# Kernel optimization log

Measured on AMD Instinct MI355X. Metric: run time of the kernel, lower is better.

Reference implementation:

```python
import jax, jax.numpy as jnp
import numpy as np
from jax import lax

OBS_LEN = 8
PRED_LEN = 12
DIM = 128      # hidden_dim
EMB = 64       # embedding_dim
HEADS = 4
MODES = 5
SCENE = 32     # peds per scene
NPED = 8192    # total peds (256 scenes)


def _lin(key, out_d, in_d):
    kw, kb = jax.random.split(key)
    w = jax.random.normal(kw, (out_d, in_d), jnp.float32) / np.sqrt(in_d).astype(np.float32)
    b = jax.random.normal(kb, (out_d,), jnp.float32) * 0.01
    return w, b


def _stack(key, n, out_d, in_d):
    ws, bs = zip(*[_lin(k, out_d, in_d) for k in jax.random.split(key, n)])
    return jnp.stack(ws), jnp.stack(bs)


def setup_inputs() -> dict:
    key = jax.random.key(0)
    ks = jax.random.split(key, 24)
    inp = {}
    inp['obs_traj'] = jax.random.normal(ks[0], (OBS_LEN, NPED, 2), jnp.float32)
    inp['pe_w'], inp['pe_b'] = _lin(ks[1], EMB, 2)
    inp['lstm_wih'], inp['lstm_bih'] = _lin(ks[2], 4 * DIM, EMB)
    inp['lstm_whh'], inp['lstm_bhh'] = _lin(ks[3], 4 * DIM, DIM)
    inp['rp_w1'], inp['rp_b1'] = _lin(ks[4], DIM // 2, 2)
    inp['rp_w2'], inp['rp_b2'] = _lin(ks[5], DIM, DIM // 2)
    inp['wq'], inp['bq'] = _lin(ks[6], DIM, DIM)
    inp['wk'], inp['bk'] = _lin(ks[7], DIM, DIM)
    inp['wv'], inp['bv'] = _lin(ks[8], DIM, DIM)
    inp['wo'], inp['bo'] = _lin(ks[9], DIM, DIM)
    inp['op_w'], inp['op_b'] = _lin(ks[10], DIM, 2 * DIM)
    inp['mp_w1'], inp['mp_b1'] = _lin(ks[11], DIM, 2 * DIM)
    inp['mp_w2'], inp['mp_b2'] = _lin(ks[12], MODES, DIM)
    inp['td_w1'], inp['td_b1'] = _stack(ks[13], MODES, DIM, 2 * DIM)
    inp['td_w2'], inp['td_b2'] = _stack(ks[14], MODES, DIM, DIM)
    inp['td_w3'], inp['td_b3'] = _stack(ks[15], MODES, PRED_LEN * 2, DIM)
    inp['ud_w1'], inp['ud_b1'] = _stack(ks[16], MODES, DIM // 2, 2 * DIM)
    inp['ud_w2'], inp['ud_b2'] = _stack(ks[17], MODES, PRED_LEN * 2, DIM // 2)
    inp['scene_size'] = SCENE
    return inp


def reference(obs_traj, pe_w, pe_b, lstm_wih, lstm_bih, lstm_whh, lstm_bhh,
              rp_w1, rp_b1, rp_w2, rp_b2, wq, bq, wk, bk, wv, bv, wo, bo,
              op_w, op_b, mp_w1, mp_b1, mp_w2, mp_b2,
              td_w1, td_b1, td_w2, td_b2, td_w3, td_b3,
              ud_w1, ud_b1, ud_w2, ud_b2, scene_size):
    obs = jnp.transpose(obs_traj, (1, 0, 2))          # (N, T, 2)
    N = obs.shape[0]
    D = lstm_whh.shape[1]

    # ---- NodeHistoryEncoder: Linear embed + 1-layer LSTM, last hidden ----
    emb = jnp.einsum('ntd,ed->nte', obs, pe_w) + pe_b  # (N, T, EMB)

    def step(carry, x):
        h, c = carry
        g = x @ lstm_wih.T + lstm_bih + h @ lstm_whh.T + lstm_bhh
        i, f, gg, o = jnp.split(g, 4, axis=-1)          # torch gate order i,f,g,o
        c = jax.nn.sigmoid(f) * c + jax.nn.sigmoid(i) * jnp.tanh(gg)
        h = jax.nn.sigmoid(o) * jnp.tanh(c)
        return (h, c), None

    h0 = jnp.zeros((N, D), obs.dtype)
    (node_features, _), _ = lax.scan(step, (h0, h0), jnp.swapaxes(emb, 0, 1))
    last_pos = obs[:, -1, :]                            # (N, 2)

    # ---- EdgeEncoder: per-scene rel-pos-biased multi-head attention ----
    S = scene_size
    B = N // S
    feat = node_features.reshape(B, S, D)
    pos = last_pos.reshape(B, S, 2)
    rel = pos[:, None, :, :] - pos[:, :, None, :]       # [b,i,j] = pos_j - pos_i
    rel_enc = jax.nn.relu(jnp.einsum('bijd,hd->bijh', rel, rp_w1) + rp_b1)
    rel_enc = jnp.einsum('bijh,eh->bije', rel_enc, rp_w2) + rp_b2  # (B,S,S,D)
    kv = feat[:, None, :, :] + rel_enc                  # key == value
    dh = D // HEADS
    q = (feat @ wq.T + bq).reshape(B, S, HEADS, dh)
    kp = (jnp.einsum('bijd,ed->bije', kv, wk) + bk).reshape(B, S, S, HEADS, dh)
    vp = (jnp.einsum('bijd,ed->bije', kv, wv) + bv).reshape(B, S, S, HEADS, dh)
    scores = jnp.einsum('bihd,bijhd->bhij', q, kp) / np.sqrt(dh).astype(np.float32)
    attn = jax.nn.softmax(scores, axis=-1)
    ctx = jnp.einsum('bhij,bijhd->bihd', attn, vp).reshape(B, S, D)
    attn_out = ctx @ wo.T + bo
    edge = (jnp.concatenate([feat, attn_out], axis=-1) @ op_w.T + op_b).reshape(N, D)

    f_all = jnp.concatenate([node_features, edge], axis=-1)  # (N, 2D)

    # ---- GMMDecoder ----
    probs = jax.nn.softmax(jax.nn.relu(f_all @ mp_w1.T + mp_b1) @ mp_w2.T + mp_b2, axis=-1)
    h1 = jax.nn.relu(jnp.einsum('nd,mhd->nmh', f_all, td_w1) + td_b1)    # (N,M,D)
    h2 = jax.nn.relu(jnp.einsum('nmh,mgh->nmg', h1, td_w2) + td_b2)
    traj = (jnp.einsum('nmg,mog->nmo', h2, td_w3) + td_b3).reshape(N, MODES, PRED_LEN, 2)
    u1 = jax.nn.relu(jnp.einsum('nd,mhd->nmh', f_all, ud_w1) + ud_b1)
    sigmas = jax.nn.softplus(jnp.einsum('nmh,moh->nmo', u1, ud_w2) + ud_b2).reshape(N, MODES, PRED_LEN, 2)
    predictions = jnp.cumsum(traj, axis=2) + last_pos[:, None, None, :]
    return predictions, probs
```

## Files before the change

### kernel.cpp

```cpp
#include <hip/hip_runtime.h>
#include <math.h>

typedef __attribute__((ext_vector_type(8))) short short8;
typedef __attribute__((ext_vector_type(4))) float f32x4;

#define NPED 8192
#define INVS 0.1767766952966369f

#define B_WHH    0
#define B_WQKV   131072
#define B_WK2PAD 229376
#define B_OPWE   294912
#define B_MPW1   360448
#define B_TDW1   425984
#define B_TDW2   753664
#define B_TDW3C  917504
#define F_WIHE   958464
#define F_BEFF   962560
#define F_WV2T   964608
#define F_BQKV   997376
#define F_BEDGE  998912
#define F_TDB3C  999424
#define F_ZERO   999936
#define A_FEAT   1000960
#define A_QKV    3098112

__device__ __forceinline__ float bf2f(ushort u) {
  union { unsigned i; float f; } v; v.i = ((unsigned)u) << 16; return v.f;
}
__device__ __forceinline__ float blo(unsigned u) {
  union { unsigned i; float f; } v; v.i = u << 16; return v.f;
}
__device__ __forceinline__ float bhi(unsigned u) {
  union { unsigned i; float f; } v; v.i = u & 0xffff0000u; return v.f;
}
__device__ __forceinline__ ushort f2bf(float f) {
  union { float f; unsigned i; } v; v.f = f;
  unsigned r = v.i + 0x7fffu + ((v.i >> 16) & 1u);
  return (ushort)(r >> 16);
}

__global__ __launch_bounds__(256) void prep(
    const float* __restrict__ wih, const float* __restrict__ bih, const float* __restrict__ bhh,
    const float* __restrict__ pew, const float* __restrict__ peb,
    const float* __restrict__ wk, const float* __restrict__ wv,
    const float* __restrict__ rpw2, const float* __restrict__ rpb2,
    const float* __restrict__ bq, const float* __restrict__ bk, const float* __restrict__ bv,
    const float* __restrict__ whh, const float* __restrict__ wq, const float* __restrict__ wo,
    const float* __restrict__ opw, const float* __restrict__ opb, const float* __restrict__ bo,
    const float* __restrict__ mpw1,
    const float* __restrict__ tdw1, const float* __restrict__ tdw2,
    const float* __restrict__ tdw3, const float* __restrict__ tdb3,
    char* __restrict__ wsb) {
  int tid = blockIdx.x * 256 + threadIdx.x;
  if (tid < 512) {
    int d = tid;
    float s0 = 0.f, s1 = 0.f, sb = 0.f;
    for (int e = 0; e < 64; ++e) {
      float w = wih[d * 64 + e];
      s0 += w * pew[e * 2]; s1 += w * pew[e * 2 + 1]; sb += w * peb[e];
    }
    ((float*)(wsb + F_WIHE))[d * 2] = s0;
    ((float*)(wsb + F_WIHE))[d * 2 + 1] = s1;
    ((float*)(wsb + F_BEFF))[d] = bih[d] + bhh[d] + sb;
  } else if (tid < 49664) {
    int j = tid - 512; int n = j >> 7, k = j & 127;
    float v = (n < 128) ? wq[n * 128 + k] * INVS
                        : (n < 256) ? wk[(n - 128) * 128 + k] : wv[(n - 256) * 128 + k];
    ((ushort*)(wsb + B_WQKV))[j] = f2bf(v);
  } else if (tid < 82432) {
    int idx = tid - 49664; int r = idx >> 7, d = idx & 127;
    int h = r >> 6, e = r & 63;
    float s = 0.f;
    if ((d >> 5) == h)
      for (int c = 0; c < 128; ++c) s += wk[d * 128 + c] * rpw2[c * 64 + e];
    ((ushort*)(wsb + B_WK2PAD))[idx] = f2bf(s);
  } else if (tid < 115200) {
    int idx = tid - 82432; int o = idx >> 8, k = idx & 255;
    float s;
    if (k < 128) s = opw[o * 256 + k];
    else {
      s = 0.f;
      for (int c = 0; c < 128; ++c) s += opw[o * 256 + 128 + c] * wo[c * 128 + (k - 128)];
    }
    ((ushort*)(wsb + B_OPWE))[idx] = f2bf(s);
  } else if (tid < 147968) {
    int j = tid - 115200; ((ushort*)(wsb + B_MPW1))[j] = f2bf(mpw1[j]);
  } else if (tid < 311808) {
    int j = tid - 147968; ((ushort*)(wsb + B_TDW1))[j] = f2bf(tdw1[j]);
  } else if (tid < 393728) {
    int j = tid - 311808; ((ushort*)(wsb + B_TDW2))[j] = f2bf(tdw2[j]);
  } else if (tid < 414208) {
    int j = tid - 393728; int m = j >> 12, r = j & 4095, o = r >> 7, k = r & 127;
    float s = 0.f;
    if (o < 24) {
      int c = o & 1, jj = o >> 1;
      for (int jp = 0; jp <= jj; ++jp) s += tdw3[(m * 24 + jp * 2 + c) * 128 + k];
    }
    ((ushort*)(wsb + B_TDW3C))[j] = f2bf(s);
  } else if (tid < 414328) {
    int j = tid - 414208; int m = j / 24, o = j % 24;
    int c = o & 1, jj = o >> 1;
    float s = 0.f;
    for (int jp = 0; jp <= jj; ++jp) s += tdb3[m * 24 + jp * 2 + c];
    ((float*)(wsb + F_TDB3C))[j] = s;
  } else if (tid < 414712) {
    int d = tid - 414328;
    float s;
    if (d < 128) s = bq[d] * INVS;
    else if (d < 256) {
      int dd = d - 128; s = bk[dd];
      for (int c = 0; c < 128; ++c) s += wk[dd * 128 + c] * rpb2[c];
    } else {
      int dd = d - 256; s = bv[dd];
      for (int c = 0; c < 128; ++c) s += wv[dd * 128 + c] * rpb2[c];
    }
    ((float*)(wsb + F_BQKV))[d] = s;
  } else if (tid < 414840) {
    int o = tid - 414712;
    float s = opb[o];
    for (int c = 0; c < 128; ++c) s += opw[o * 256 + 128 + c] * bo[c];
    ((float*)(wsb + F_BEDGE))[o] = s;
  } else if (tid < 415096) {
    ((float*)(wsb + F_ZERO))[tid - 414840] = 0.f;
  } else if (tid < 423288) {
    int idx = tid - 415096; int e = idx >> 7, hd = idx & 127;
    float s = 0.f;
    for (int c = 0; c < 128; ++c) s += wv[hd * 128 + c] * rpw2[c * 64 + e];
    ((float*)(wsb + F_WV2T))[idx] = s;
  } else if (tid < 488824) {
    int i = tid - 423288;
    ((ushort*)(wsb + B_WHH))[i] = f2bf(whh[i]);
  }
}

__global__ __launch_bounds__(512) void lstm_mfma(
    const float* __restrict__ obs, const ushort* __restrict__ whhb,
    const float* __restrict__ wihe, const float* __restrict__ beff,
    ushort* __restrict__ feat) {
  __shared__ ushort Hs[32 * 128];
  __shared__ float obs_s[8][32][2];
  int tid = threadIdx.x;
  int w = tid >> 6, l = tid & 63;
  int lm = l & 15, lg = l >> 4;
  int nb = blockIdx.x * 32;
  {
    int ts = tid >> 6, p = (tid >> 1) & 31, c = tid & 1;
    obs_s[ts][p][c] = obs[ts * (NPED * 2) + (nb + p) * 2 + c];
  }
  for (int i = tid; i < 4096; i += 512) Hs[i] = 0;
  short8 bfr[4][4];
  float wx0[4], wx1[4], be[4];
#pragma unroll
  for (int q = 0; q < 4; ++q) {
    int g = q * 128 + w * 16 + lm;
    wx0[q] = wihe[g * 2]; wx1[q] = wihe[g * 2 + 1]; be[q] = beff[g];
#pragma unroll
    for (int ks = 0; ks < 4; ++ks)
      bfr[q][ks] = *(const short8*)(const void*)&whhb[g * 128 + ks * 32 + lg * 8];
  }
  float cst[2][4] = {};
  __syncthreads();
  for (int ts = 0; ts < 8; ++ts) {
    f32x4 acc[2][4];
#pragma unroll
    for (int mi = 0; mi < 2; ++mi)
#pragma unroll
      for (int r = 0; r < 4; ++r) {
        int p = mi * 16 + lg * 4 + r;
        float ox = obs_s[ts][p][0], oy = obs_s[ts][p][1];
#pragma unroll
        for (int q = 0; q < 4; ++q)
          acc[mi][q][r] = be[q] + wx0[q] * ox + wx1[q] * oy;
      }
#pragma unroll
    for (int ks = 0; ks < 4; ++ks) {
      int p0 = lm, p1 = 16 + lm;
      short8 a0 = *(const short8*)(const void*)&Hs[p0 * 128 + ((ks * 32 + lg * 8) ^ ((p0 & 7) << 3))];
      short8 a1 = *(const short8*)(const void*)&Hs[p1 * 128 + ((ks * 32 + lg * 8) ^ ((p1 & 7) << 3))];
#pragma unroll
      for (int q = 0; q < 4; ++q) {
        acc[0][q] = __builtin_amdgcn_mfma_f32_16x16x32_bf16(a0, bfr[q][ks], acc[0][q], 0, 0, 0);
        acc[1][q] = __builtin_amdgcn_mfma_f32_16x16x32_bf16(a1, bfr[q][ks], acc[1][q], 0, 0, 0);
      }
    }
    __syncthreads();
    int d = w * 16 + lm;
#pragma unroll
    for (int mi = 0; mi < 2; ++mi)
#pragma unroll
      for (int r = 0; r < 4; ++r) {
        int p = mi * 16 + lg * 4 + r;
        float xi = acc[mi][0][r], xf = acc[mi][1][r], xg = acc[mi][2][r], xo = acc[mi][3][r];
        float ig = 1.f / (1.f + __expf(-xi));
        float fg = 1.f / (1.f + __expf(-xf));
        xg = fminf(fmaxf(xg, -30.f), 30.f);
        float eg = __expf(-2.f * xg);
        float gg = (1.f - eg) / (1.f + eg);
        float og = 1.f / (1.f + __expf(-xo));
        float cv = fg * cst[mi][r] + ig * gg;
        cst[mi][r] = cv;
        float cvc = fminf(fmaxf(cv, -30.f), 30.f);
        float ec = __expf(-2.f * cvc);
        float th = (1.f - ec) / (1.f + ec);
        ushort hb = f2bf(og * th);
        Hs[p * 128 + (d ^ ((p & 7) << 3))] = hb;
        if (ts == 7) feat[(size_t)(nb + p) * 128 + d] = hb;
      }
    __syncthreads();
  }
}

template<int NF, int NKS, int K1KS>
__global__ __launch_bounds__(256) void mfma_gemm(
    const ushort* __restrict__ A1, int lda1,
    const ushort* __restrict__ A2, int lda2,
    const ushort* __restrict__ Bw,
    const float* __restrict__ bias,
    ushort* __restrict__ out, int ldo, int ooff, int relu) {
  int w = threadIdx.x >> 6, l = threadIdx.x & 63;
  int lm = l & 15, lg = l >> 4;
  int row = blockIdx.x * 64 + w * 16 + lm;
  int col0 = blockIdx.y * (NF * 16);
  f32x4 acc[NF];
#pragma unroll
  for (int i = 0; i < NF; ++i) acc[i] = (f32x4){0.f, 0.f, 0.f, 0.f};
#pragma unroll
  for (int ks = 0; ks < NKS; ++ks) {
    int kb = ks * 32 + lg * 8;
    const ushort* ap = (ks < K1KS) ? (A1 + (size_t)row * lda1 + kb)
                                   : (A2 + (size_t)row * lda2 + (kb - K1KS * 32));
    short8 af = *(const short8*)(const void*)ap;
#pragma unroll
    for (int ni = 0; ni < NF; ++ni) {
      short8 bf = *(const short8*)(const void*)(Bw + (size_t)(col0 + ni * 16 + lm) * (NKS * 32) + kb);
      acc[ni] = __builtin_amdgcn_mfma_f32_16x16x32_bf16(af, bf, acc[ni], 0, 0, 0);
    }
  }
  int orow0 = blockIdx.x * 64 + w * 16 + lg * 4;
#pragma unroll
  for (int ni = 0; ni < NF; ++ni) {
    int c = col0 + ni * 16 + lm;
    float bv = bias[c];
#pragma unroll
    for (int r = 0; r < 4; ++r) {
      float v = acc[ni][r] + bv;
      if (relu) v = fmaxf(v, 0.f);
      out[(size_t)(orow0 + r) * ldo + ooff + c] = f2bf(v);
    }
  }
}

__global__ __launch_bounds__(256) void mp_probs(
    const ushort* __restrict__ feat, const ushort* __restrict__ qkv,
    const ushort* __restrict__ w1b, const float* __restrict__ mpb1,
    const float* __restrict__ mpw2, const float* __restrict__ mpb2,
    float* __restrict__ out) {
  __shared__ float w2s[5][128];
  int t = threadIdx.x;
  for (int i = t; i < 640; i += 256) w2s[i >> 7][i & 127] = mpw2[i];
  __syncthreads();
  int w = t >> 6, l = t & 63, lm = l & 15, lg = l >> 4;
  int row = blockIdx.x * 64 + w * 16 + lm;
  f32x4 acc[8];
#pragma unroll
  for (int i = 0; i < 8; ++i) acc[i] = (f32x4){0.f, 0.f, 0.f, 0.f};
#pragma unroll
  for (int ks = 0; ks < 8; ++ks) {
    int kb = ks * 32 + lg * 8;
    const ushort* ap = (ks < 4) ? (feat + (size_t)row * 128 + kb)
                                : (qkv + (size_t)row * 640 + 256 + (kb - 128));
    short8 af = *(const short8*)(const void*)ap;
#pragma unroll
    for (int ni = 0; ni < 8; ++ni) {
      short8 bf = *(const short8*)(const void*)(w1b + (size_t)(ni * 16 + lm) * 256 + kb);
      acc[ni] = __builtin_amdgcn_mfma_f32_16x16x32_bf16(af, bf, acc[ni], 0, 0, 0);
    }
  }
  float bc[8];
#pragma unroll
  for (int ni = 0; ni < 8; ++ni) bc[ni] = mpb1[ni * 16 + lm];
  float lgt[4][5];
#pragma unroll
  for (int r = 0; r < 4; ++r)
#pragma unroll
    for (int m = 0; m < 5; ++m) {
      float s = 0.f;
#pragma unroll
      for (int ni = 0; ni < 8; ++ni)
        s += fmaxf(acc[ni][r] + bc[ni], 0.f) * w2s[m][ni * 16 + lm];
      lgt[r][m] = s;
    }
#pragma unroll
  for (int mask = 1; mask < 16; mask <<= 1)
#pragma unroll
    for (int r = 0; r < 4; ++r)
#pragma unroll
      for (int m = 0; m < 5; ++m)
        lgt[r][m] += __shfl_xor(lgt[r][m], mask);
  if (lm < 5) {
#pragma unroll
    for (int r = 0; r < 4; ++r) {
      float b0 = lgt[r][0] + mpb2[0];
      float mx = b0;
      float lv[5]; lv[0] = b0;
#pragma unroll
      for (int m = 1; m < 5; ++m) { lv[m] = lgt[r][m] + mpb2[m]; mx = fmaxf(mx, lv[m]); }
      float sm = 0.f;
#pragma unroll
      for (int m = 0; m < 5; ++m) { lv[m] = expf(lv[m] - mx); sm += lv[m]; }
      int n = blockIdx.x * 64 + w * 16 + lg * 4 + r;
      out[983040 + (size_t)n * 5 + lm] = lv[lm] / sm;
    }
  }
}

__global__ __launch_bounds__(256) void td_fused(
    const ushort* __restrict__ feat, const ushort* __restrict__ qkv,
    const ushort* __restrict__ w1b, const float* __restrict__ tdb1,
    const ushort* __restrict__ w2b, const float* __restrict__ tdb2,
    const ushort* __restrict__ w3c, const float* __restrict__ b3c,
    const float* __restrict__ obs, float* __restrict__ out) {
  __shared__ ushort slab[64 * 136];
  int t = threadIdx.x, w = t >> 6, l = t & 63, lm = l & 15, lg = l >> 4;
  int m = blockIdx.y;
  int row = blockIdx.x * 64 + w * 16 + lm;
  const ushort* W1 = w1b + (size_t)m * 32768;
  const ushort* W2 = w2b + (size_t)m * 16384;
  const ushort* W3 = w3c + (size_t)m * 4096;
  const float* B1 = tdb1 + m * 128;
  const float* B2 = tdb2 + m * 128;
  f32x4 a1[8];
#pragma unroll
  for (int i = 0; i < 8; ++i) a1[i] = (f32x4){0.f, 0.f, 0.f, 0.f};
#pragma unroll
  for (int ks = 0; ks < 8; ++ks) {
    int kb = ks * 32 + lg * 8;
    const ushort* ap = (ks < 4) ? (feat + (size_t)row * 128 + kb)
                                : (qkv + (size_t)row * 640 + 256 + (kb - 128));
    short8 af = *(const short8*)(const void*)ap;
#pragma unroll
    for (int ni = 0; ni < 8; ++ni) {
      short8 bf = *(const short8*)(const void*)(W1 + (size_t)(ni * 16 + lm) * 256 + kb);
      a1[ni] = __builtin_amdgcn_mfma_f32_16x16x32_bf16(af, bf, a1[ni], 0, 0, 0);
    }
  }
#pragma unroll
  for (int ni = 0; ni < 8; ++ni) {
    float bb = B1[ni * 16 + lm];
#pragma unroll
    for (int r = 0; r < 4; ++r)
      slab[(w * 16 + lg * 4 + r) * 136 + ni * 16 + lm] = f2bf(fmaxf(a1[ni][r] + bb, 0.f));
  }
  __syncthreads();
  short8 af2[4];
#pragma unroll
  for (int ks = 0; ks < 4; ++ks)
    af2[ks] = *(const short8*)(const void*)&slab[(w * 16 + lm) * 136 + ks * 32 + lg * 8];
  f32x4 a2[8];
#pragma unroll
  for (int i = 0; i < 8; ++i) a2[i] = (f32x4){0.f, 0.f, 0.f, 0.f};
#pragma unroll
  for (int ks = 0; ks < 4; ++ks) {
    int kb = ks * 32 + lg * 8;
#pragma unroll
    for (int ni = 0; ni < 8; ++ni) {
      short8 bf = *(const short8*)(const void*)(W2 + (size_t)(ni * 16 + lm) * 128 + kb);
      a2[ni] = __builtin_amdgcn_mfma_f32_16x16x32_bf16(af2[ks], bf, a2[ni], 0, 0, 0);
    }
  }
  __syncthreads();
#pragma unroll
  for (int ni = 0; ni < 8; ++ni) {
    float bb = B2[ni * 16 + lm];
#pragma unroll
    for (int r = 0; r < 4; ++r)
      slab[(w * 16 + lg * 4 + r) * 136 + ni * 16 + lm] = f2bf(fmaxf(a2[ni][r] + bb, 0.f));
  }
  __syncthreads();
  short8 af3[4];
#pragma unroll
  for (int ks = 0; ks < 4; ++ks)
    af3[ks] = *(const short8*)(const void*)&slab[(w * 16 + lm) * 136 + ks * 32 + lg * 8];
  f32x4 a3[2];
  a3[0] = (f32x4){0.f, 0.f, 0.f, 0.f}; a3[1] = (f32x4){0.f, 0.f, 0.f, 0.f};
#pragma unroll
  for (int ks = 0; ks < 4; ++ks) {
    int kb = ks * 32 + lg * 8;
#pragma unroll
    for (int ni = 0; ni < 2; ++ni) {
      short8 bf = *(const short8*)(const void*)(W3 + (size_t)(ni * 16 + lm) * 128 + kb);
      a3[ni] = __builtin_amdgcn_mfma_f32_16x16x32_bf16(af3[ks], bf, a3[ni], 0, 0, 0);
    }
  }
#pragma unroll
  for (int ni = 0; ni < 2; ++ni) {
    int o = ni * 16 + lm;
    if (o < 24) {
      float bb = b3c[m * 24 + o];
      int c = o & 1;
#pragma unroll
      for (int r = 0; r < 4; ++r) {
        int n = blockIdx.x * 64 + w * 16 + lg * 4 + r;
        out[(size_t)n * 120 + m * 24 + o] = a3[ni][r] + bb + obs[7 * (NPED * 2) + n * 2 + c];
      }
    }
  }
}

__global__ __launch_bounds__(256) void attn_kernel(
    const float* __restrict__ obs, ushort* QKV,
    const float* __restrict__ wv2T,
    const float* __restrict__ rpw1, const float* __restrict__ rpb1) {
  __shared__ ushort K0s[32 * 128];
  __shared__ ushort V0s[32 * 128];
  __shared__ ushort renc[4 * 32 * 64];
  __shared__ float Qi[4][128];
  __shared__ float QWs[4][256];
  __shared__ float att[4][4][32];
  __shared__ float AR[4][4][64];
  __shared__ float rpx[64], rpy[64], rpb[64];
  __shared__ float posS[32][2];
  __shared__ float posI[4][2];
  int t = threadIdx.x;
  int scene = blockIdx.x & 255, ic = blockIdx.x >> 8;
  int i0 = ic * 4, sbase = scene * 32;

  for (int idx = t; idx < 1024; idx += 256) {
    int arr = idx >> 9, j = (idx >> 4) & 31, c = idx & 15;
    short8 v = *(const short8*)(const void*)&QKV[(size_t)(sbase + j) * 640 + 128 + arr * 128 + c * 8];
    ushort* dst = arr ? V0s : K0s;
    *(short8*)(void*)&dst[j * 128 + (c ^ (j & 7)) * 8] = v;
  }
  for (int idx = t; idx < 512; idx += 256) {
    int ii = idx >> 7, d = idx & 127;
    Qi[ii][d] = bf2f(QKV[(size_t)(sbase + i0 + ii) * 640 + d]);
  }
  for (int idx = t; idx < 1024; idx += 256) {
    int ii = idx >> 8, e = idx & 255;
    QWs[ii][e] = bf2f(QKV[(size_t)(sbase + i0 + ii) * 640 + 384 + e]);
  }
  if (t < 64) posS[t >> 1][t & 1] = obs[7 * (NPED * 2) + (sbase + (t >> 1)) * 2 + (t & 1)];
  else if (t < 72) {
    int q = t - 64;
    posI[q >> 1][q & 1] = obs[7 * (NPED * 2) + (sbase + i0 + (q >> 1)) * 2 + (q & 1)];
  } else if (t >= 128 && t < 192) {
    int e = t - 128;
    rpx[e] = rpw1[e * 2]; rpy[e] = rpw1[e * 2 + 1]; rpb[e] = rpb1[e];
  }
  __syncthreads();

  for (int idx = t; idx < 1024; idx += 256) {
    int ii = idx >> 8, j = (idx >> 3) & 31, c = idx & 7;
    float dx = posS[j][0] - posI[ii][0], dy = posS[j][1] - posI[ii][1];
    short8 pk;
#pragma unroll
    for (int r = 0; r < 8; ++r) {
      int e = c * 8 + r;
      pk[r] = (short)f2bf(fmaxf(rpx[e] * dx + rpy[e] * dy + rpb[e], 0.f));
    }
    *(short8*)(void*)&renc[(ii * 32 + j) * 64 + (c ^ (j & 7)) * 8] = pk;
  }
  __syncthreads();

  for (int idx = t; idx < 512; idx += 256) {
    int ii = idx >> 7, h = (idx >> 5) & 3, j = idx & 31;
    float s = 0.f;
#pragma unroll
    for (int cc = 0; cc < 4; ++cc) {
      uint4 kv = *(const uint4*)(const void*)&K0s[j * 128 + (((h * 4 + cc) ^ (j & 7)) * 8)];
      const float4 qa = *(const float4*)&Qi[ii][h * 32 + cc * 8];
      const float4 qb = *(const float4*)&Qi[ii][h * 32 + cc * 8 + 4];
      s += blo(kv.x) * qa.x + bhi(kv.x) * qa.y + blo(kv.y) * qa.z + bhi(kv.y) * qa.w;
      s += blo(kv.z) * qb.x + bhi(kv.z) * qb.y + blo(kv.w) * qb.z + bhi(kv.w) * qb.w;
    }
#pragma unroll
    for (int c = 0; c < 8; ++c) {
      uint4 rv = *(const uint4*)(const void*)&renc[(ii * 32 + j) * 64 + ((c ^ (j & 7)) * 8)];
      const float4 ua = *(const float4*)&QWs[ii][h * 64 + c * 8];
      const float4 ub = *(const float4*)&QWs[ii][h * 64 + c * 8 + 4];
      s += blo(rv.x) * ua.x + bhi(rv.x) * ua.y + blo(rv.y) * ua.z + bhi(rv.y) * ua.w;
      s += blo(rv.z) * ub.x + bhi(rv.z) * ub.y + blo(rv.w) * ub.z + bhi(rv.w) * ub.w;
    }
    att[ii][h][j] = s;
  }
  __syncthreads();

  {
    int r = t >> 4, lj = t & 15;
    float v0 = att[r >> 2][r & 3][lj], v1 = att[r >> 2][r & 3][lj + 16];
    float mx = fmaxf(v0, v1);
    mx = fmaxf(mx, __shfl_xor(mx, 8, 16));
    mx = fmaxf(mx, __shfl_xor(mx, 4, 16));
    mx = fmaxf(mx, __shfl_xor(mx, 2, 16));
    mx = fmaxf(mx, __shfl_xor(mx, 1, 16));
    float e0 = expf(v0 - mx), e1 = expf(v1 - mx);
    float sm = e0 + e1;
    sm += __shfl_xor(sm, 8, 16);
    sm += __shfl_xor(sm, 4, 16);
    sm += __shfl_xor(sm, 2, 16);
    sm += __shfl_xor(sm, 1, 16);
    float inv = 1.f / sm;
    att[r >> 2][r & 3][lj] = e0 * inv;
    att[r >> 2][r & 3][lj + 16] = e1 * inv;
  }
  __syncthreads();

  {
    int ii = t >> 6, h = (t >> 4) & 3, e4 = t & 15;
    int c = e4 >> 1, off = (e4 & 1) * 4;
    float a0 = 0.f, a1 = 0.f, a2 = 0.f, a3 = 0.f;
    for (int j = 0; j < 32; ++j) {
      float av = att[ii][h][j];
      uint2 rv = *(const uint2*)(const void*)&renc[(ii * 32 + j) * 64 + ((c ^ (j & 7)) * 8) + off];
      a0 += av * blo(rv.x); a1 += av * bhi(rv.x);
      a2 += av * blo(rv.y); a3 += av * bhi(rv.y);
    }
    *(float4*)&AR[ii][h][e4 * 4] = make_float4(a0, a1, a2, a3);
  }
  __syncthreads();

  {
    int ii = t >> 6, l = t & 63;
    int h5 = l >> 5, hd4 = l & 31;
    int hd = hd4 * 4, h = hd >> 5;
    float c0 = 0.f, c1 = 0.f, c2 = 0.f, c3 = 0.f;
    int cch = hd >> 3, offh = hd & 7;
    for (int j = h5 * 16; j < h5 * 16 + 16; ++j) {
      float av = att[ii][h][j];
      uint2 vv = *(const uint2*)(const void*)&V0s[j * 128 + ((cch ^ (j & 7)) * 8) + offh];
      c0 += av * blo(vv.x); c1 += av * bhi(vv.x);
      c2 += av * blo(vv.y); c3 += av * bhi(vv.y);
    }
    for (int e4 = h5 * 8; e4 < h5 * 8 + 8; ++e4) {
      const float4 ar = *(const float4*)&AR[ii][h][e4 * 4];
#pragma unroll
      for (int r = 0; r < 4; ++r) {
        const float4 wv = *(const float4*)&wv2T[(e4 * 4 + r) * 128 + hd];
        float a = (r == 0) ? ar.x : (r == 1) ? ar.y : (r == 2) ? ar.z : ar.w;
        c0 += a * wv.x; c1 += a * wv.y; c2 += a * wv.z; c3 += a * wv.w;
      }
    }
    c0 += __shfl_xor(c0, 32); c1 += __shfl_xor(c1, 32);
    c2 += __shfl_xor(c2, 32); c3 += __shfl_xor(c3, 32);
    if (h5 == 0) {
      ushort4 o;
      o.x = f2bf(c0); o.y = f2bf(c1); o.z = f2bf(c2); o.w = f2bf(c3);
      *(ushort4*)(void*)&QKV[(size_t)(sbase + i0 + ii) * 640 + hd] = o;
    }
  }
}

extern "C" void kernel_launch(void* const* d_in, const int* in_sizes, int n_in,
                              void* d_out, int out_size, void* d_ws, size_t ws_size,
                              hipStream_t stream) {
  (void)in_sizes; (void)n_in; (void)out_size; (void)ws_size;
  const float* obs  = (const float*)d_in[0];
  const float* pew  = (const float*)d_in[1];
  const float* peb  = (const float*)d_in[2];
  const float* wih  = (const float*)d_in[3];
  const float* bih  = (const float*)d_in[4];
  const float* whh  = (const float*)d_in[5];
  const float* bhh  = (const float*)d_in[6];
  const float* rpw1 = (const float*)d_in[7];
  const float* rpb1 = (const float*)d_in[8];
  const float* rpw2 = (const float*)d_in[9];
  const float* rpb2 = (const float*)d_in[10];
  const float* wq   = (const float*)d_in[11];
  const float* bq   = (const float*)d_in[12];
  const float* wk   = (const float*)d_in[13];
  const float* bk   = (const float*)d_in[14];
  const float* wv   = (const float*)d_in[15];
  const float* bv   = (const float*)d_in[16];
  const float* wo   = (const float*)d_in[17];
  const float* bo   = (const float*)d_in[18];
  const float* opw  = (const float*)d_in[19];
  const float* opb  = (const float*)d_in[20];
  const float* mpw1 = (const float*)d_in[21];
  const float* mpb1 = (const float*)d_in[22];
  const float* mpw2 = (const float*)d_in[23];
  const float* mpb2 = (const float*)d_in[24];
  const float* tdw1 = (const float*)d_in[25];
  const float* tdb1 = (const float*)d_in[26];
  const float* tdw2 = (const float*)d_in[27];
  const float* tdb2 = (const float*)d_in[28];
  const float* tdw3 = (const float*)d_in[29];
  const float* tdb3 = (const float*)d_in[30];
  char* wsb = (char*)d_ws;
  float* out = (float*)d_out;

  ushort* whhb   = (ushort*)(wsb + B_WHH);
  ushort* wqkvb  = (ushort*)(wsb + B_WQKV);
  ushort* wk2pb  = (ushort*)(wsb + B_WK2PAD);
  ushort* opweb  = (ushort*)(wsb + B_OPWE);
  ushort* mpw1b  = (ushort*)(wsb + B_MPW1);
  ushort* tdw1b  = (ushort*)(wsb + B_TDW1);
  ushort* tdw2b  = (ushort*)(wsb + B_TDW2);
  ushort* tdw3cb = (ushort*)(wsb + B_TDW3C);
  ushort* featb  = (ushort*)(wsb + A_FEAT);
  ushort* qkvb   = (ushort*)(wsb + A_QKV);

  prep<<<1910, 256, 0, stream>>>(wih, bih, bhh, pew, peb, wk, wv, rpw2, rpb2,
                                 bq, bk, bv, whh, wq, wo, opw, opb, bo, mpw1,
                                 tdw1, tdw2, tdw3, tdb3, wsb);
  lstm_mfma<<<256, 512, 0, stream>>>(obs, whhb, (float*)(wsb + F_WIHE),
                                     (float*)(wsb + F_BEFF), featb);
  mfma_gemm<4, 4, 4><<<dim3(128, 6), 256, 0, stream>>>(
      featb, 128, featb, 128, wqkvb, (float*)(wsb + F_BQKV), qkvb, 640, 0, 0);
  mfma_gemm<4, 4, 4><<<dim3(128, 4), 256, 0, stream>>>(
      qkvb, 640, qkvb, 640, wk2pb, (float*)(wsb + F_ZERO), qkvb, 640, 384, 0);
  attn_kernel<<<2048, 256, 0, stream>>>(obs, qkvb, (float*)(wsb + F_WV2T), rpw1, rpb1);
  mfma_gemm<4, 8, 4><<<dim3(128, 2), 256, 0, stream>>>(
      featb, 128, qkvb, 640, opweb, (float*)(wsb + F_BEDGE), qkvb, 640, 256, 0);
  mp_probs<<<128, 256, 0, stream>>>(featb, qkvb, mpw1b, mpb1, mpw2, mpb2, out);
  td_fused<<<dim3(128, 5), 256, 0, stream>>>(featb, qkvb, tdw1b, tdb1, tdw2b, tdb2,
                                             tdw3cb, (float*)(wsb + F_TDB3C), obs, out);
}
```

Before: 276.4 us.

## Fold key projection into QKV weights, prefetch B fragments, split mp_probs columns

Precomputes the product of the padded key-projection weight with wq (scaled) in a new prep2 kernel, so the QKV GEMM emits the projected-query columns directly and the second dependent GEMM launch is dropped. All MFMA GEMM loops now load the A fragments up front and double-buffer the weight fragments per k-step. mp_probs splits the 128 hidden columns across wave pairs with an LDS reduction and launches twice as many blocks. This trades an extra small prep kernel and more register pressure for one fewer launch and better latency hiding.

```diff
diff --git a/kernel.cpp b/kernel.cpp
--- a/kernel.cpp
+++ b/kernel.cpp
@@ -9,21 +9,20 @@
 
 #define B_WHH    0
 #define B_WQKV   131072
-#define B_WK2PAD 229376
-#define B_OPWE   294912
-#define B_MPW1   360448
-#define B_TDW1   425984
-#define B_TDW2   753664
-#define B_TDW3C  917504
-#define F_WIHE   958464
-#define F_BEFF   962560
-#define F_WV2T   964608
-#define F_BQKV   997376
-#define F_BEDGE  998912
-#define F_TDB3C  999424
-#define F_ZERO   999936
-#define A_FEAT   1000960
-#define A_QKV    3098112
+#define B_WK2PAD 294912
+#define B_OPWE   360448
+#define B_MPW1   425984
+#define B_TDW1   491520
+#define B_TDW2   819200
+#define B_TDW3C  983040
+#define F_WIHE   1024000
+#define F_BEFF   1028096
+#define F_WV2T   1030144
+#define F_BQKV   1062912
+#define F_BEDGE  1065472
+#define F_TDB3C  1065984
+#define A_FEAT   1066496
+#define A_QKV    3163648
 
 __device__ __forceinline__ float bf2f(ushort u) {
   union { unsigned i; float f; } v; v.i = ((unsigned)u) << 16; return v.f;
@@ -104,25 +103,23 @@
     float s = 0.f;
     for (int jp = 0; jp <= jj; ++jp) s += tdb3[m * 24 + jp * 2 + c];
     ((float*)(wsb + F_TDB3C))[j] = s;
-  } else if (tid < 414712) {
+  } else if (tid < 414968) {
     int d = tid - 414328;
-    float s;
+    float s = 0.f;
     if (d < 128) s = bq[d] * INVS;
     else if (d < 256) {
       int dd = d - 128; s = bk[dd];
       for (int c = 0; c < 128; ++c) s += wk[dd * 128 + c] * rpb2[c];
-    } else {
+    } else if (d < 384) {
       int dd = d - 256; s = bv[dd];
       for (int c = 0; c < 128; ++c) s += wv[dd * 128 + c] * rpb2[c];
     }
     ((float*)(wsb + F_BQKV))[d] = s;
-  } else if (tid < 414840) {
-    int o = tid - 414712;
+  } else if (tid < 415096) {
+    int o = tid - 414968;
     float s = opb[o];
     for (int c = 0; c < 128; ++c) s += opw[o * 256 + 128 + c] * bo[c];
     ((float*)(wsb + F_BEDGE))[o] = s;
-  } else if (tid < 415096) {
-    ((float*)(wsb + F_ZERO))[tid - 414840] = 0.f;
   } else if (tid < 423288) {
     int idx = tid - 415096; int e = idx >> 7, hd = idx & 127;
     float s = 0.f;
@@ -131,6 +128,29 @@
   } else if (tid < 488824) {
     int i = tid - 423288;
     ((ushort*)(wsb + B_WHH))[i] = f2bf(whh[i]);
+  }
+}
+
+__global__ __launch_bounds__(256) void prep2(
+    const ushort* __restrict__ wk2pad, const float* __restrict__ wq,
+    const float* __restrict__ bq, ushort* __restrict__ wqkv, float* __restrict__ bqkv) {
+  int idx = blockIdx.x * 256 + threadIdx.x;
+  if (idx < 32768) {
+    int e = idx >> 7, k = idx & 127, h = e >> 6;
+    float s = 0.f;
+    for (int dd = 0; dd < 32; ++dd) {
+      int d = h * 32 + dd;
+      s += bf2f(wk2pad[e * 128 + d]) * wq[d * 128 + k];
+    }
+    wqkv[(384 + e) * 128 + k] = f2bf(s * INVS);
+  } else if (idx < 33024) {
+    int e = idx - 32768, h = e >> 6;
+    float s = 0.f;
+    for (int dd = 0; dd < 32; ++dd) {
+      int d = h * 32 + dd;
+      s += bf2f(wk2pad[e * 128 + d]) * bq[d];
+    }
+    bqkv[384 + e] = s * INVS;
   }
 }
 
@@ -225,17 +245,29 @@
   f32x4 acc[NF];
 #pragma unroll
   for (int i = 0; i < NF; ++i) acc[i] = (f32x4){0.f, 0.f, 0.f, 0.f};
+  short8 afA[NKS];
 #pragma unroll
   for (int ks = 0; ks < NKS; ++ks) {
-    int kb = ks * 32 + lg * 8;
-    const ushort* ap = (ks < K1KS) ? (A1 + (size_t)row * lda1 + kb)
-                                   : (A2 + (size_t)row * lda2 + (kb - K1KS * 32));
-    short8 af = *(const short8*)(const void*)ap;
-#pragma unroll
-    for (int ni = 0; ni < NF; ++ni) {
-      short8 bf = *(const short8*)(const void*)(Bw + (size_t)(col0 + ni * 16 + lm) * (NKS * 32) + kb);
-      acc[ni] = __builtin_amdgcn_mfma_f32_16x16x32_bf16(af, bf, acc[ni], 0, 0, 0);
-    }
+    const ushort* ap = (ks < K1KS) ? (A1 + (size_t)row * lda1 + ks * 32 + lg * 8)
+                                   : (A2 + (size_t)row * lda2 + (ks - K1KS) * 32 + lg * 8);
+    afA[ks] = *(const short8*)(const void*)ap;
+  }
+  short8 bA[NF], bB[NF];
+#pragma unroll
+  for (int ni = 0; ni < NF; ++ni)
+    bA[ni] = *(const short8*)(const void*)(Bw + (size_t)(col0 + ni * 16 + lm) * (NKS * 32) + lg * 8);
+#pragma unroll
+  for (int ks = 0; ks < NKS; ++ks) {
+    short8* cur = (ks & 1) ? bB : bA;
+    short8* nxt = (ks & 1) ? bA : bB;
+    if (ks + 1 < NKS) {
+#pragma unroll
+      for (int ni = 0; ni < NF; ++ni)
+        nxt[ni] = *(const short8*)(const void*)(Bw + (size_t)(col0 + ni * 16 + lm) * (NKS * 32) + (ks + 1) * 32 + lg * 8);
+    }
+#pragma unroll
+    for (int ni = 0; ni < NF; ++ni)
+      acc[ni] = __builtin_amdgcn_mfma_f32_16x16x32_bf16(afA[ks], cur[ni], acc[ni], 0, 0, 0);
   }
   int orow0 = blockIdx.x * 64 + w * 16 + lg * 4;
 #pragma unroll
@@ -257,29 +289,43 @@
     const float* __restrict__ mpw2, const float* __restrict__ mpb2,
     float* __restrict__ out) {
   __shared__ float w2s[5][128];
+  __shared__ float pc[2][16][5];
   int t = threadIdx.x;
   for (int i = t; i < 640; i += 256) w2s[i >> 7][i & 127] = mpw2[i];
-  __syncthreads();
   int w = t >> 6, l = t & 63, lm = l & 15, lg = l >> 4;
-  int row = blockIdx.x * 64 + w * 16 + lm;
-  f32x4 acc[8];
-#pragma unroll
-  for (int i = 0; i < 8; ++i) acc[i] = (f32x4){0.f, 0.f, 0.f, 0.f};
+  int g = w >> 1, ch = w & 1, cb = ch * 64;
+  int row = blockIdx.x * 32 + g * 16 + lm;
+  f32x4 acc[4];
+#pragma unroll
+  for (int i = 0; i < 4; ++i) acc[i] = (f32x4){0.f, 0.f, 0.f, 0.f};
+  short8 afA[8];
 #pragma unroll
   for (int ks = 0; ks < 8; ++ks) {
-    int kb = ks * 32 + lg * 8;
-    const ushort* ap = (ks < 4) ? (feat + (size_t)row * 128 + kb)
-                                : (qkv + (size_t)row * 640 + 256 + (kb - 128));
-    short8 af = *(const short8*)(const void*)ap;
-#pragma unroll
-    for (int ni = 0; ni < 8; ++ni) {
-      short8 bf = *(const short8*)(const void*)(w1b + (size_t)(ni * 16 + lm) * 256 + kb);
-      acc[ni] = __builtin_amdgcn_mfma_f32_16x16x32_bf16(af, bf, acc[ni], 0, 0, 0);
-    }
-  }
-  float bc[8];
-#pragma unroll
-  for (int ni = 0; ni < 8; ++ni) bc[ni] = mpb1[ni * 16 + lm];
+    const ushort* ap = (ks < 4) ? (feat + (size_t)row * 128 + ks * 32 + lg * 8)
+                                : (qkv + (size_t)row * 640 + 256 + (ks - 4) * 32 + lg * 8);
+    afA[ks] = *(const short8*)(const void*)ap;
+  }
+  short8 bA[4], bB[4];
+#pragma unroll
+  for (int ni = 0; ni < 4; ++ni)
+    bA[ni] = *(const short8*)(const void*)(w1b + (size_t)(cb + ni * 16 + lm) * 256 + lg * 8);
+#pragma unroll
+  for (int ks = 0; ks < 8; ++ks) {
+    short8* cur = (ks & 1) ? bB : bA;
+    short8* nxt = (ks & 1) ? bA : bB;
+    if (ks + 1 < 8) {
+#pragma unroll
+      for (int ni = 0; ni < 4; ++ni)
+        nxt[ni] = *(const short8*)(const void*)(w1b + (size_t)(cb + ni * 16 + lm) * 256 + (ks + 1) * 32 + lg * 8);
+    }
+#pragma unroll
+    for (int ni = 0; ni < 4; ++ni)
+      acc[ni] = __builtin_amdgcn_mfma_f32_16x16x32_bf16(afA[ks], cur[ni], acc[ni], 0, 0, 0);
+  }
+  __syncthreads();
+  float bc[4];
+#pragma unroll
+  for (int ni = 0; ni < 4; ++ni) bc[ni] = mpb1[cb + ni * 16 + lm];
   float lgt[4][5];
 #pragma unroll
   for (int r = 0; r < 4; ++r)
@@ -287,8 +333,8 @@
     for (int m = 0; m < 5; ++m) {
       float s = 0.f;
 #pragma unroll
-      for (int ni = 0; ni < 8; ++ni)
-        s += fmaxf(acc[ni][r] + bc[ni], 0.f) * w2s[m][ni * 16 + lm];
+      for (int ni = 0; ni < 4; ++ni)
+        s += fmaxf(acc[ni][r] + bc[ni], 0.f) * w2s[m][cb + ni * 16 + lm];
       lgt[r][m] = s;
     }
 #pragma unroll
@@ -298,18 +344,23 @@
 #pragma unroll
       for (int m = 0; m < 5; ++m)
         lgt[r][m] += __shfl_xor(lgt[r][m], mask);
-  if (lm < 5) {
+  if (ch == 1 && lm < 5) {
+#pragma unroll
+    for (int r = 0; r < 4; ++r) pc[g][lg * 4 + r][lm] = lgt[r][lm];
+  }
+  __syncthreads();
+  if (ch == 0 && lm < 5) {
 #pragma unroll
     for (int r = 0; r < 4; ++r) {
-      float b0 = lgt[r][0] + mpb2[0];
-      float mx = b0;
-      float lv[5]; lv[0] = b0;
-#pragma unroll
-      for (int m = 1; m < 5; ++m) { lv[m] = lgt[r][m] + mpb2[m]; mx = fmaxf(mx, lv[m]); }
-      float sm = 0.f;
+      float lv[5], mx = -1e30f, sm = 0.f;
+#pragma unroll
+      for (int m = 0; m < 5; ++m) {
+        lv[m] = lgt[r][m] + pc[g][lg * 4 + r][m] + mpb2[m];
+        mx = fmaxf(mx, lv[m]);
+      }
 #pragma unroll
       for (int m = 0; m < 5; ++m) { lv[m] = expf(lv[m] - mx); sm += lv[m]; }
-      int n = blockIdx.x * 64 + w * 16 + lg * 4 + r;
+      int n = blockIdx.x * 32 + g * 16 + lg * 4 + r;
       out[983040 + (size_t)n * 5 + lm] = lv[lm] / sm;
     }
   }
@@ -330,19 +381,33 @@
   const ushort* W3 = w3c + (size_t)m * 4096;
   const float* B1 = tdb1 + m * 128;
   const float* B2 = tdb2 + m * 128;
+  short8 afA[8];
+#pragma unroll
+  for (int ks = 0; ks < 8; ++ks) {
+    const ushort* ap = (ks < 4) ? (feat + (size_t)row * 128 + ks * 32 + lg * 8)
+                                : (qkv + (size_t)row * 640 + 256 + (ks - 4) * 32 + lg * 8);
+    afA[ks] = *(const short8*)(const void*)ap;
+  }
   f32x4 a1[8];
 #pragma unroll
   for (int i = 0; i < 8; ++i) a1[i] = (f32x4){0.f, 0.f, 0.f, 0.f};
-#pragma unroll
-  for (int ks = 0; ks < 8; ++ks) {
-    int kb = ks * 32 + lg * 8;
-    const ushort* ap = (ks < 4) ? (feat + (size_t)row * 128 + kb)
-                                : (qkv + (size_t)row * 640 + 256 + (kb - 128));
-    short8 af = *(const short8*)(const void*)ap;
-#pragma unroll
-    for (int ni = 0; ni < 8; ++ni) {
-      short8 bf = *(const short8*)(const void*)(W1 + (size_t)(ni * 16 + lm) * 256 + kb);
-      a1[ni] = __builtin_amdgcn_mfma_f32_16x16x32_bf16(af, bf, a1[ni], 0, 0, 0);
+  {
+    short8 bA[8], bB[8];
+#pragma unroll
+    for (int ni = 0; ni < 8; ++ni)
+      bA[ni] = *(const short8*)(const void*)(W1 + (size_t)(ni * 16 + lm) * 256 + lg * 8);
+#pragma unroll
+    for (int ks = 0; ks < 8; ++ks) {
+      short8* cur = (ks & 1) ? bB : bA;
+      short8* nxt = (ks & 1) ? bA : bB;
+      if (ks + 1 < 8) {
+#pragma unroll
+        for (int ni = 0; ni < 8; ++ni)
+          nxt[ni] = *(const short8*)(const void*)(W1 + (size_t)(ni * 16 + lm) * 256 + (ks + 1) * 32 + lg * 8);
+      }
+#pragma unroll
+      for (int ni = 0; ni < 8; ++ni)
+        a1[ni] = __builtin_amdgcn_mfma_f32_16x16x32_bf16(afA[ks], cur[ni], a1[ni], 0, 0, 0);
     }
   }
 #pragma unroll
@@ -360,13 +425,23 @@
   f32x4 a2[8];
 #pragma unroll
   for (int i = 0; i < 8; ++i) a2[i] = (f32x4){0.f, 0.f, 0.f, 0.f};
-#pragma unroll
-  for (int ks = 0; ks < 4; ++ks) {
-    int kb = ks * 32 + lg * 8;
-#pragma unroll
-    for (int ni = 0; ni < 8; ++ni) {
-      short8 bf = *(const short8*)(const void*)(W2 + (size_t)(ni * 16 + lm) * 128 + kb);
-      a2[ni] = __builtin_amdgcn_mfma_f32_16x16x32_bf16(af2[ks], bf, a2[ni], 0, 0, 0);
+  {
+    short8 bA[8], bB[8];
+#pragma unroll
+    for (int ni = 0; ni < 8; ++ni)
+      bA[ni] = *(const short8*)(const void*)(W2 + (size_t)(ni * 16 + lm) * 128 + lg * 8);
+#pragma unroll
+    for (int ks = 0; ks < 4; ++ks) {
+      short8* cur = (ks & 1) ? bB : bA;
+      short8* nxt = (ks & 1) ? bA : bB;
+      if (ks + 1 < 4) {
+#pragma unroll
+        for (int ni = 0; ni < 8; ++ni)
+          nxt[ni] = *(const short8*)(const void*)(W2 + (size_t)(ni * 16 + lm) * 128 + (ks + 1) * 32 + lg * 8);
+      }
+#pragma unroll
+      for (int ni = 0; ni < 8; ++ni)
+        a2[ni] = __builtin_amdgcn_mfma_f32_16x16x32_bf16(af2[ks], cur[ni], a2[ni], 0, 0, 0);
     }
   }
   __syncthreads();
@@ -378,6 +453,12 @@
       slab[(w * 16 + lg * 4 + r) * 136 + ni * 16 + lm] = f2bf(fmaxf(a2[ni][r] + bb, 0.f));
   }
   __syncthreads();
+  short8 w3f[2][4];
+#pragma unroll
+  for (int ni = 0; ni < 2; ++ni)
+#pragma unroll
+    for (int ks = 0; ks < 4; ++ks)
+      w3f[ni][ks] = *(const short8*)(const void*)(W3 + (size_t)(ni * 16 + lm) * 128 + ks * 32 + lg * 8);
   short8 af3[4];
 #pragma unroll
   for (int ks = 0; ks < 4; ++ks)
@@ -385,14 +466,10 @@
   f32x4 a3[2];
   a3[0] = (f32x4){0.f, 0.f, 0.f, 0.f}; a3[1] = (f32x4){0.f, 0.f, 0.f, 0.f};
 #pragma unroll
-  for (int ks = 0; ks < 4; ++ks) {
-    int kb = ks * 32 + lg * 8;
-#pragma unroll
-    for (int ni = 0; ni < 2; ++ni) {
-      short8 bf = *(const short8*)(const void*)(W3 + (size_t)(ni * 16 + lm) * 128 + kb);
-      a3[ni] = __builtin_amdgcn_mfma_f32_16x16x32_bf16(af3[ks], bf, a3[ni], 0, 0, 0);
-    }
-  }
+  for (int ks = 0; ks < 4; ++ks)
+#pragma unroll
+    for (int ni = 0; ni < 2; ++ni)
+      a3[ni] = __builtin_amdgcn_mfma_f32_16x16x32_bf16(af3[ks], w3f[ni][ks], a3[ni], 0, 0, 0);
 #pragma unroll
   for (int ni = 0; ni < 2; ++ni) {
     int o = ni * 16 + lm;
@@ -603,16 +680,15 @@
   prep<<<1910, 256, 0, stream>>>(wih, bih, bhh, pew, peb, wk, wv, rpw2, rpb2,
                                  bq, bk, bv, whh, wq, wo, opw, opb, bo, mpw1,
                                  tdw1, tdw2, tdw3, tdb3, wsb);
+  prep2<<<129, 256, 0, stream>>>(wk2pb, wq, bq, wqkvb, (float*)(wsb + F_BQKV));
   lstm_mfma<<<256, 512, 0, stream>>>(obs, whhb, (float*)(wsb + F_WIHE),
                                      (float*)(wsb + F_BEFF), featb);
-  mfma_gemm<4, 4, 4><<<dim3(128, 6), 256, 0, stream>>>(
+  mfma_gemm<4, 4, 4><<<dim3(128, 10), 256, 0, stream>>>(
       featb, 128, featb, 128, wqkvb, (float*)(wsb + F_BQKV), qkvb, 640, 0, 0);
-  mfma_gemm<4, 4, 4><<<dim3(128, 4), 256, 0, stream>>>(
-      qkvb, 640, qkvb, 640, wk2pb, (float*)(wsb + F_ZERO), qkvb, 640, 384, 0);
   attn_kernel<<<2048, 256, 0, stream>>>(obs, qkvb, (float*)(wsb + F_WV2T), rpw1, rpb1);
   mfma_gemm<4, 8, 4><<<dim3(128, 2), 256, 0, stream>>>(
       featb, 128, qkvb, 640, opweb, (float*)(wsb + F_BEDGE), qkvb, 640, 256, 0);
-  mp_probs<<<128, 256, 0, stream>>>(featb, qkvb, mpw1b, mpb1, mpw2, mpb2, out);
+  mp_probs<<<256, 256, 0, stream>>>(featb, qkvb, mpw1b, mpb1, mpw2, mpb2, out);
   td_fused<<<dim3(128, 5), 256, 0, stream>>>(featb, qkvb, tdw1b, tdb1, tdw2b, tdb2,
                                              tdw3cb, (float*)(wsb + F_TDB3C), obs, out);
 }
```

Result: no change. 272.2 us (-1.5%).
